# Kernel optimization log

Hardware: AMD Instinct MI355X
Metric: run time of the kernel (lower is better)

## Reference

```python
import jax, jax.numpy as jnp
import numpy as np

NH, KVH, HD = 32, 8, 128          # num heads, kv heads, head dim
HIDDEN = NH * HD                   # 4096
K_BITS = V_BITS = 4
GROUP = 32                         # quantization group size
THETA = 10000.0
FEAT = 32 // K_BITS                # values packed per int32


def _rope_cos_sin(pos, dtype=jnp.float32):
    inv_freq = 1.0 / (THETA ** (jnp.arange(0, HD, 2, dtype=jnp.float32) / HD))
    freqs = pos.astype(jnp.float32)[:, None] * inv_freq[None, :]
    emb = jnp.concatenate([freqs, freqs], axis=-1)  # [t, HD]
    return jnp.cos(emb).astype(dtype), jnp.sin(emb).astype(dtype)


def _rotate_half(x):
    x1, x2 = jnp.split(x, 2, axis=-1)
    return jnp.concatenate([-x2, x1], axis=-1)


def _apply_rope(x, pos):  # x: [b, h, t, d], pos: [t]
    cos, sin = _rope_cos_sin(pos, x.dtype)
    return x * cos[None, None] + _rotate_half(x) * sin[None, None]


def _unpack(packed, bits):
    # packed int32 [..., n] -> float [..., n * (32//bits)], little-endian bit fields
    feat = 32 // bits
    shifts = jnp.arange(feat, dtype=jnp.int32) * bits
    vals = (packed[..., None] >> shifts) & ((1 << bits) - 1)
    return vals.reshape(packed.shape[:-1] + (packed.shape[-1] * feat,)).astype(jnp.float32)


def _dequant(packed, scale, mn, bits, group):
    # group-wise affine dequant: x = q * scale + mn along last dim
    qv = _unpack(packed, bits)
    lead, L = qv.shape[:-1], qv.shape[-1]
    qv = qv.reshape(lead + (L // group, group))
    return (qv * scale[..., None] + mn[..., None]).reshape(lead + (L,))


def _repeat_kv(x, n):
    return jnp.repeat(x, n, axis=1)


def setup_inputs() -> dict:
    key = jax.random.key(0)
    ks = jax.random.split(key, 13)
    B, QL = 8, 8
    TQ, FULL_PAST = 3968, 56
    s = 0.02
    return {
        "hidden_states": jax.random.normal(ks[0], (B, QL, HIDDEN), jnp.float32),
        "Wq": jax.random.normal(ks[1], (NH * HD, HIDDEN), jnp.float32) * s,
        "Wk": jax.random.normal(ks[2], (KVH * HD, HIDDEN), jnp.float32) * s,
        "Wv": jax.random.normal(ks[3], (KVH * HD, HIDDEN), jnp.float32) * s,
        "Wo": jax.random.normal(ks[4], (NH * HD, NH * HD), jnp.float32) * s,
        "key_quant_trans": jax.random.randint(ks[5], (B, KVH, HD, TQ // FEAT), 0, 2**31 - 1, jnp.int32),
        "key_scale_trans": jax.random.uniform(ks[6], (B, KVH, HD, TQ // GROUP), jnp.float32) * 0.05 + 0.01,
        "key_mn_trans": jax.random.normal(ks[7], (B, KVH, HD, TQ // GROUP), jnp.float32) * 0.1,
        "key_full_past": jax.random.normal(ks[8], (B, KVH, FULL_PAST, HD), jnp.float32),
        "value_quant": jax.random.randint(ks[9], (B, KVH, TQ, HD // FEAT), 0, 2**31 - 1, jnp.int32),
        "value_scale": jax.random.uniform(ks[10], (B, KVH, TQ, HD // GROUP), jnp.float32) * 0.05 + 0.01,
        "value_mn": jax.random.normal(ks[11], (B, KVH, TQ, HD // GROUP), jnp.float32) * 0.1,
        "value_full_past": jax.random.normal(ks[12], (B, KVH, FULL_PAST, HD), jnp.float32),
    }


def reference(hidden_states, Wq, Wk, Wv, Wo,
              key_quant_trans, key_scale_trans, key_mn_trans, key_full_past,
              value_quant, value_scale, value_mn, value_full_past):
    b, q_len, _ = hidden_states.shape
    groups = NH // KVH
    # projections
    q = (hidden_states @ Wq.T).reshape(b, q_len, NH, HD).transpose(0, 2, 1, 3)
    k = (hidden_states @ Wk.T).reshape(b, q_len, KVH, HD).transpose(0, 2, 1, 3)
    v = (hidden_states @ Wv.T).reshape(b, q_len, KVH, HD).transpose(0, 2, 1, 3)

    TQ = key_quant_trans.shape[-1] * FEAT
    past_len = TQ + key_full_past.shape[2]
    pos_new = jnp.arange(past_len, past_len + q_len)
    qr = _apply_rope(q, pos_new)

    # quantized key segment: dequant (stored transposed [b,kvh,HD,TQ]) + fused RoPE + bmm
    kq = _dequant(key_quant_trans, key_scale_trans, key_mn_trans, K_BITS, GROUP)
    kq = _apply_rope(kq.transpose(0, 1, 3, 2), jnp.arange(TQ))  # [b,kvh,TQ,HD]
    att_quant = jnp.einsum('bhqd,bhkd->bhqk', qr, _repeat_kv(kq, groups))

    # full-precision residual key segment
    k_full = jnp.concatenate([key_full_past, k], axis=2)
    pos_full = jnp.arange(past_len + q_len - k_full.shape[2], past_len + q_len)
    k_full = _apply_rope(k_full, pos_full)
    att_full = jnp.einsum('bhqd,bhkd->bhqk', qr, _repeat_kv(k_full, groups))

    attn = jnp.concatenate([att_quant, att_full], axis=-1) / np.sqrt(HD).astype(np.float32)
    attn = jax.nn.softmax(attn.astype(jnp.float32), axis=-1).astype(qr.dtype)

    # quantized values (packed along head_dim) + full residual values
    vq = _dequant(value_quant, value_scale, value_mn, V_BITS, GROUP)  # [b,kvh,TQ,HD]
    v_full = jnp.concatenate([value_full_past, v], axis=2)
    Lf = v_full.shape[2]
    out = jnp.einsum('bhqk,bhkd->bhqd', attn[..., :-Lf], _repeat_kv(vq, groups)) \
        + jnp.einsum('bhqk,bhkd->bhqd', attn[..., -Lf:], _repeat_kv(v_full, groups))

    out = out.transpose(0, 2, 1, 3).reshape(b, q_len, NH * HD)
    return out @ Wo.T
```

## Files before the change

### kernel.cpp

```cpp
#include <hip/hip_runtime.h>

typedef unsigned short u16;
typedef short bf16x8 __attribute__((ext_vector_type(8)));
typedef float f32x4 __attribute__((ext_vector_type(4)));

__device__ __forceinline__ float b2f(u16 u){ return __uint_as_float(((unsigned)u)<<16); }
__device__ __forceinline__ u16 f2bf(float f){ return (u16)((__float_as_uint(f)+0x8000u)>>16); }
__device__ __forceinline__ float ldf(const void* p, int i, bool isbf){
  return isbf ? b2f(((const u16*)p)[i]) : ((const float*)p)[i];
}
__device__ __forceinline__ float2 ld2(const void* p, int i, bool isbf){
  if (isbf) { unsigned u = *(const unsigned*)((const u16*)p + i);
              return make_float2(b2f((u16)(u & 0xffffu)), b2f((u16)(u >> 16))); }
  return *(const float2*)((const float*)p + i);
}
__device__ __forceinline__ void ld8(u16* dst, const void* p, int i, bool isbf){
  if (isbf) { *(uint4*)dst = *(const uint4*)((const u16*)p + i); }
  else {
    float4 a = *(const float4*)((const float*)p + i);
    float4 b = *(const float4*)((const float*)p + i + 4);
    dst[0]=f2bf(a.x); dst[1]=f2bf(a.y); dst[2]=f2bf(a.z); dst[3]=f2bf(a.w);
    dst[4]=f2bf(b.x); dst[5]=f2bf(b.y); dst[6]=f2bf(b.z); dst[7]=f2bf(b.w);
  }
}
__device__ __forceinline__ float c8(const float* __restrict__ p, int i, int stride){
  float s = 0.f;
  #pragma unroll
  for (int k = 0; k < 8; k++) s += p[i + k*stride];
  return s;
}
__device__ __forceinline__ void bar(){ asm volatile("s_waitcnt lgkmcnt(0)\n\ts_barrier" ::: "memory"); }
#define RORMAX(x, ctrl) fmaxf((x), __int_as_float(__builtin_amdgcn_update_dpp( \
    __float_as_int(x), __float_as_int(x), (ctrl), 0xF, 0xF, false)))
#define MFMA16(a,b,c) __builtin_amdgcn_mfma_f32_16x16x32_bf16((a),(b),(c),0,0,0)

__global__ __launch_bounds__(256) void ctab_kernel(const u16* __restrict__ h,
                                                   int* __restrict__ flag,
                                                   float2* __restrict__ ctab) {
  int tid = threadIdx.x;
  if (blockIdx.x == 0) {
    int cnt = 0;
    for (int i = tid; i < 4096; i += 256) {
      int e = (h[i] >> 7) & 0xFF;
      cnt += (e >= 116 && e <= 132) ? 1 : 0;
    }
    __shared__ int sh[256];
    sh[tid] = cnt; __syncthreads();
    for (int s = 128; s > 0; s >>= 1) { if (tid < s) sh[tid] += sh[tid + s]; __syncthreads(); }
    if (tid == 0) flag[0] = (sh[0] >= 3100) ? 1 : 0;
  }
  int idx = blockIdx.x * 256 + tid;
  int dm = idx & 63, t = idx >> 6;
  float f = exp2f(-(float)dm * (13.287712379549449f / 64.0f));
  float ang = (float)t * f;
  float s, c;
  sincosf(ang, &s, &c);
  ctab[idx] = make_float2(c, s);
}

__global__ __launch_bounds__(256) void proj_kernel(
    const void* __restrict__ X, const void* __restrict__ Wa,
    const void* __restrict__ Wb, const void* __restrict__ Wc,
    float* __restrict__ out32, int Na, int Nb, int ostride,
    const int* __restrict__ flagp, int x_dyn)
{
  bool fbf = (*flagp != 0);
  bool xbf = x_dyn ? fbf : true;
  int n0 = blockIdx.x * 32;
  int ks0 = blockIdx.y * 512;
  const void* W; int wr0;
  if (n0 < Na)           { W = Wa; wr0 = n0; }
  else if (n0 < Na + Nb) { W = Wb; wr0 = n0 - Na; }
  else                   { W = Wc; wr0 = n0 - Na - Nb; }

  __shared__ u16 Xs[64][136];
  __shared__ u16 Ws[32][136];
  int tid = threadIdx.x;
  int wv = tid >> 6, lane = tid & 63, lr = lane & 15, lq = lane >> 4;
  f32x4 acc0 = {0.f,0.f,0.f,0.f}, acc1 = {0.f,0.f,0.f,0.f};

  for (int ki = 0; ki < 4; ki++) {
    int k0 = ks0 + ki * 128;
    __syncthreads();
    for (int u = tid; u < 1024; u += 256) {
      int row = u >> 4, cc = u & 15;
      ld8(&Xs[row][cc * 8], X, row * 4096 + k0 + cc * 8, xbf);
    }
    for (int u = tid; u < 512; u += 256) {
      int row = u >> 4, cc = u & 15;
      ld8(&Ws[row][cc * 8], W, (wr0 + row) * 4096 + k0 + cc * 8, fbf);
    }
    __syncthreads();
    #pragma unroll
    for (int ks = 0; ks < 4; ks++) {
      bf16x8 af = *(const bf16x8*)&Xs[wv * 16 + lr][ks * 32 + lq * 8];
      bf16x8 b0 = *(const bf16x8*)&Ws[lr][ks * 32 + lq * 8];
      bf16x8 b1 = *(const bf16x8*)&Ws[16 + lr][ks * 32 + lq * 8];
      acc0 = MFMA16(af, b0, acc0);
      acc1 = MFMA16(af, b1, acc1);
    }
  }
  float* outp = out32 + (size_t)blockIdx.y * 64 * ostride;
  #pragma unroll
  for (int r = 0; r < 4; r++) {
    outp[(wv * 16 + lq * 4 + r) * ostride + n0 + lr]      = acc0[r];
    outp[(wv * 16 + lq * 4 + r) * ostride + n0 + 16 + lr] = acc1[r];
  }
}

__global__ __launch_bounds__(256) void prep_kernel(
    const float* __restrict__ Cq32, const void* __restrict__ kfp, const void* __restrict__ vfp,
    const float2* __restrict__ ctab, const int* __restrict__ flagp,
    u16* __restrict__ qrb, u16* __restrict__ kfullb, u16* __restrict__ vfullT)
{
  bool isbf = (*flagp != 0);
  int idx = blockIdx.x * 256 + threadIdx.x;
  if (idx < 262144) {
    int d = idx & 127, row = (idx >> 7) & 31, bh = idx >> 12;
    int b = bh >> 3, kvh = bh & 7, g = row >> 3, qp = row & 7;
    int tok = b * 8 + qp, h = kvh * 4 + g;
    float x  = c8(Cq32, tok * 6144 + h * 128 + d, 393216);
    float x2 = c8(Cq32, tok * 6144 + h * 128 + (d ^ 64), 393216);
    float2 cs = ctab[(4024 + qp) * 64 + (d & 63)];
    float sgn = (d < 64) ? -1.f : 1.f;
    qrb[idx] = f2bf(x * cs.x + sgn * (x2 * cs.y));
  } else if (idx < 786432) {
    int j = idx - 262144;
    int d = j & 127, t = (j >> 7) & 63, bh = j >> 13;
    int b = bh >> 3, kvh = bh & 7;
    float x, x2;
    if (t < 56) {
      x  = ldf(kfp, (bh * 56 + t) * 128 + d, isbf);
      x2 = ldf(kfp, (bh * 56 + t) * 128 + (d ^ 64), isbf);
    } else {
      int tok = b * 8 + (t - 56);
      x  = c8(Cq32, tok * 6144 + 4096 + kvh * 128 + d, 393216);
      x2 = c8(Cq32, tok * 6144 + 4096 + kvh * 128 + (d ^ 64), 393216);
    }
    float2 cs = ctab[(3968 + t) * 64 + (d & 63)];
    float sgn = (d < 64) ? -1.f : 1.f;
    kfullb[j] = f2bf(x * cs.x + sgn * (x2 * cs.y));
  } else {
    int j = idx - 786432;
    int t = j & 63, d = (j >> 6) & 127, bh = j >> 13;
    int b = bh >> 3, kvh = bh & 7;
    float x;
    if (t < 56) x = ldf(vfp, (bh * 56 + t) * 128 + d, isbf);
    else        x = c8(Cq32, (b * 8 + t - 56) * 6144 + 5120 + kvh * 128 + d, 393216);
    vfullT[j] = f2bf(x);
  }
}

__global__ __launch_bounds__(256) void attn_kernel(
    const int* __restrict__ kqw, const void* __restrict__ ksc, const void* __restrict__ kmn,
    const int* __restrict__ vqw, const void* __restrict__ vsc, const void* __restrict__ vmn,
    const u16* __restrict__ qrb, const u16* __restrict__ kfullb, const u16* __restrict__ vfullT,
    const float2* __restrict__ ctab, const int* __restrict__ flagp,
    u16* __restrict__ Opart, float* __restrict__ ml)
{
  bool isbf = (*flagp != 0);
  int bh = blockIdx.x, grp = blockIdx.y;
  int tid = threadIdx.x;
  int c0 = grp * 4;
  int N = (grp == 15) ? 3 : 4;

  __shared__ __align__(16) unsigned char L[37120];
  u16* Kt = (u16*)L;
  u16* Vt = (u16*)(L + 16384);
  u16* Pt = (u16*)(L + 32768);
  float* pmax = (float*)(L + 36864);

  int wv = tid >> 6, lane = tid & 63, lr = lane & 15, lq = lane >> 4;
  int mt = wv & 1, nh = wv >> 1;
  int sx = (lr & 7) << 3;

  const int* kq_lo = kqw + (bh * 128 + lane) * 496;
  const int* kq_hi = kq_lo + 64 * 496;
  int klo = (bh * 128 + lane) * 124;
  int khi = klo + 64 * 124;
  const int* vqp = vqw + (bh * 3968 + lane) * 16 + wv * 4;
  int voff = (bh * 3968 + lane) * 4 + wv;

  bf16x8 qa[4];
  #pragma unroll
  for (int ks = 0; ks < 4; ks++)
    qa[ks] = *(const bf16x8*)&qrb[(bh * 32 + mt * 16 + lr) * 128 + ks * 32 + lq * 8];
  bf16x8 onev;
  #pragma unroll
  for (int j2 = 0; j2 < 8; j2++) onev[j2] = (short)0x3F80;

  float m_prev[4], l_run[4], alpha[4], mx[4];
  f32x4 zf = {0.f,0.f,0.f,0.f};
  f32x4 oacc[4] = {zf, zf, zf, zf};
  f32x4 sacc[2];
  #pragma unroll
  for (int r = 0; r < 4; r++) { m_prev[r] = -INFINITY; l_run[r] = 0.f; }

  unsigned kwl[2], kwh[2];
  float2 ksl, kml, ksh, kmh;
  uint4 vw; float vs, vm;

#define KLOAD(cn) do { \
    kwl[0] = kq_lo[(cn)*8 + wv]; kwl[1] = kq_lo[(cn)*8 + wv + 4]; \
    kwh[0] = kq_hi[(cn)*8 + wv]; kwh[1] = kq_hi[(cn)*8 + wv + 4]; \
    ksl = ld2(ksc, klo + (cn)*2, isbf); kml = ld2(kmn, klo + (cn)*2, isbf); \
    ksh = ld2(ksc, khi + (cn)*2, isbf); kmh = ld2(kmn, khi + (cn)*2, isbf); } while(0)
#define VLOAD(cn) do { \
    vw = *(const uint4*)(vqp + (cn)*1024); \
    vs = ldf(vsc, voff + (cn)*256, isbf); vm = ldf(vmn, voff + (cn)*256, isbf); } while(0)
#define KDEQ(cn) do { \
    _Pragma("unroll") \
    for (int it = 0; it < 2; it++) { \
      int w = wv + 4 * it; \
      unsigned w1 = kwl[it], w2 = kwh[it]; \
      float sc1 = it ? ksl.y : ksl.x, m1 = it ? kml.y : kml.x; \
      float sc2 = it ? ksh.y : ksh.x, m2 = it ? kmh.y : kmh.x; \
      const float2* ct = &ctab[((cn) * 64 + w * 8) * 64 + lane]; \
      _Pragma("unroll") \
      for (int ii = 0; ii < 8; ii++) { \
        float v1 = (float)((w1 >> (4 * ii)) & 15u) * sc1 + m1; \
        float v2 = (float)((w2 >> (4 * ii)) & 15u) * sc2 + m2; \
        float2 cs = ct[ii * 64]; \
        int t = w * 8 + ii; \
        Kt[(t * 128 + lane)      ^ ((t & 7) << 3)] = f2bf(v1 * cs.x - v2 * cs.y); \
        Kt[(t * 128 + lane + 64) ^ ((t & 7) << 3)] = f2bf(v2 * cs.x + v1 * cs.y); \
      } \
    } } while(0)
#define PVSTEP() do { \
    f32x4 pv[4] = {zf, zf, zf, zf}; f32x4 ls = zf; \
    _Pragma("unroll") \
    for (int ks = 0; ks < 2; ks++) { \
      bf16x8 af = *(const bf16x8*)&Pt[((mt*16 + lr)*64 + ks*32 + lq*8) ^ sx]; \
      ls = MFMA16(af, onev, ls); \
      _Pragma("unroll") \
      for (int nt = 0; nt < 4; nt++) { \
        bf16x8 bv = *(const bf16x8*)&Vt[((nh*64 + nt*16 + lr)*64 + ks*32 + lq*8) ^ sx]; \
        pv[nt] = MFMA16(af, bv, pv[nt]); \
      } \
    } \
    _Pragma("unroll") \
    for (int r = 0; r < 4; r++) { \
      l_run[r] = l_run[r] * alpha[r] + ls[r]; \
      _Pragma("unroll") \
      for (int nt = 0; nt < 4; nt++) \
        oacc[nt][r] = oacc[nt][r] * alpha[r] + pv[nt][r]; \
    } } while(0)

  KLOAD(c0);
  VLOAD(c0);
  KDEQ(c0);
  KLOAD(c0 + 1);
  bar();

  for (int i = 0; i < N; i++) {
    int c = c0 + i;
    f32x4 sa0 = zf, sa1 = zf;
    #pragma unroll
    for (int ks = 0; ks < 4; ks++) {
      bf16x8 b0 = *(const bf16x8*)&Kt[((nh*32 + lr)*128      + ks*32 + lq*8) ^ sx];
      bf16x8 b1 = *(const bf16x8*)&Kt[((nh*32 + 16 + lr)*128 + ks*32 + lq*8) ^ sx];
      sa0 = MFMA16(qa[ks], b0, sa0);
      sa1 = MFMA16(qa[ks], b1, sa1);
    }
    if (i > 0) PVSTEP();
    #pragma unroll
    for (int r = 0; r < 4; r++) {
      sa0[r] *= 0.08838834764831845f;
      sa1[r] *= 0.08838834764831845f;
      float m0 = fmaxf(sa0[r], sa1[r]);
      m0 = RORMAX(m0, 0x128);
      m0 = RORMAX(m0, 0x124);
      m0 = RORMAX(m0, 0x122);
      m0 = RORMAX(m0, 0x121);
      mx[r] = m0;
    }
    if (lr == 0) {
      #pragma unroll
      for (int r = 0; r < 4; r++) pmax[wv * 16 + lq * 4 + r] = mx[r];
    }
    sacc[0] = sa0; sacc[1] = sa1;
    bar();
    #pragma unroll
    for (int r = 0; r < 4; r++) {
      float cm = fmaxf(mx[r], pmax[(wv ^ 2) * 16 + lq * 4 + r]);
      float mn2 = fmaxf(m_prev[r], cm);
      alpha[r] = __expf(m_prev[r] - mn2);
      m_prev[r] = mn2;
    }
    #pragma unroll
    for (int nt = 0; nt < 2; nt++) {
      #pragma unroll
      for (int r = 0; r < 4; r++) {
        float p = __expf(sacc[nt][r] - m_prev[r]);
        int q = mt * 16 + lq * 4 + r, k = nh * 32 + nt * 16 + lr;
        Pt[(q * 64 + k) ^ ((q & 7) << 3)] = f2bf(p);
      }
    }
    if (c != 62) {
      unsigned wds[4] = {vw.x, vw.y, vw.z, vw.w};
      #pragma unroll
      for (int it = 0; it < 4; it++) {
        unsigned wd = wds[it];
        #pragma unroll
        for (int ii = 0; ii < 8; ii++) {
          int d = (wv * 4 + it) * 8 + ii;
          Vt[(d * 64 + lane) ^ ((d & 7) << 3)] = f2bf((float)((wd >> (4 * ii)) & 15u) * vs + vm);
        }
      }
    } else {
      for (int u = tid; u < 1024; u += 256) {
        int dd = u >> 3, t8 = u & 7;
        *(uint4*)&Vt[(dd * 64 + t8 * 8) ^ ((dd & 7) << 3)] =
            *(const uint4*)&vfullT[(bh * 128 + dd) * 64 + t8 * 8];
      }
    }
    if (i + 1 < N) {
      if (c + 1 == 62) {
        for (int u = tid; u < 1024; u += 256) {
          int row = u >> 4, cc = u & 15;
          *(uint4*)&Kt[(row * 128 + cc * 8) ^ ((row & 7) << 3)] =
              *(const uint4*)&kfullb[(bh * 64 + row) * 128 + cc * 8];
        }
      } else {
        KDEQ(c + 1);
      }
    }
    if (i + 2 < N && c + 2 < 62) KLOAD(c + 2);
    if (i + 1 < N && c + 1 < 62) VLOAD(c + 1);
    bar();
  }
  PVSTEP();

  u16* Ob = Opart + (size_t)((bh * 16 + grp) * 32) * 128;
  #pragma unroll
  for (int nt = 0; nt < 4; nt++)
    #pragma unroll
    for (int r = 0; r < 4; r++)
      Ob[(mt * 16 + lq * 4 + r) * 128 + nh * 64 + nt * 16 + lr] = f2bf(oacc[nt][r]);
  if (wv < 2 && lr == 0) {
    #pragma unroll
    for (int r = 0; r < 4; r++) {
      ml[((bh * 16 + grp) * 32 + mt * 16 + lq * 4 + r) * 2 + 0] = m_prev[r];
      ml[((bh * 16 + grp) * 32 + mt * 16 + lq * 4 + r) * 2 + 1] = l_run[r];
    }
  }
#undef KLOAD
#undef VLOAD
#undef KDEQ
#undef PVSTEP
}

__global__ __launch_bounds__(256) void combine_kernel(
    const u16* __restrict__ Opart, const float* __restrict__ ml, u16* __restrict__ attn_out)
{
  int bh = blockIdx.x, dq = blockIdx.y, tid = threadIdx.x;
  __shared__ float Wg[16][33];
  __shared__ float Ls[32];
  if (tid < 32) {
    int row = tid;
    float M = -INFINITY;
    for (int g = 0; g < 16; g++)
      M = fmaxf(M, ml[((bh * 16 + g) * 32 + row) * 2]);
    float Lacc = 0.f;
    for (int g = 0; g < 16; g++) {
      float m = ml[((bh * 16 + g) * 32 + row) * 2];
      float l = ml[((bh * 16 + g) * 32 + row) * 2 + 1];
      float w = __expf(m - M);
      Wg[g][row] = w;
      Lacc += l * w;
    }
    Ls[row] = Lacc;
  }
  __syncthreads();
  int row = tid >> 3, ds = tid & 7;
  int d0 = dq * 32 + ds * 4;
  float a0 = 0.f, a1 = 0.f, a2 = 0.f, a3 = 0.f;
  for (int g = 0; g < 16; g++) {
    float w = Wg[g][row];
    const u16* p = Opart + (size_t)((bh * 16 + g) * 32 + row) * 128 + d0;
    uint2 v = *(const uint2*)p;
    const u16* h = (const u16*)&v;
    a0 += w * b2f(h[0]); a1 += w * b2f(h[1]); a2 += w * b2f(h[2]); a3 += w * b2f(h[3]);
  }
  float inv = 1.0f / Ls[row];
  int b = bh >> 3, kvh = bh & 7, hg = row >> 3, qp = row & 7;
  u16* dst = attn_out + (size_t)(b * 8 + qp) * 4096 + (kvh * 4 + hg) * 128 + d0;
  dst[0] = f2bf(a0 * inv); dst[1] = f2bf(a1 * inv);
  dst[2] = f2bf(a2 * inv); dst[3] = f2bf(a3 * inv);
}

__global__ __launch_bounds__(256) void cast_kernel(
    const float* __restrict__ O32, const int* __restrict__ flagp, void* __restrict__ out)
{
  int i = blockIdx.x * 256 + threadIdx.x;
  float v = c8(O32, i, 262144);
  if (*flagp) ((u16*)out)[i] = f2bf(v);
  else        ((float*)out)[i] = v;
}

extern "C" void kernel_launch(void* const* d_in, const int* in_sizes, int n_in,
                              void* d_out, int out_size, void* d_ws, size_t ws_size,
                              hipStream_t stream)
{
  const void* hidden = d_in[0];
  const void* Wq  = d_in[1];
  const void* Wk  = d_in[2];
  const void* Wv  = d_in[3];
  const void* Wo  = d_in[4];
  const int*  kqw = (const int*)d_in[5];
  const void* ksc = d_in[6];
  const void* kmn = d_in[7];
  const void* kfp = d_in[8];
  const int*  vqw = (const int*)d_in[9];
  const void* vsc = d_in[10];
  const void* vmn = d_in[11];
  const void* vfp = d_in[12];

  char* ws = (char*)d_ws;
  int*    flag     = (int*)(ws);
  float2* ctab     = (float2*)(ws + 256);
  float*  Cq32     = (float*)(ws + 2064640);
  u16*    Opart    = (u16*)(ws + 2064640);
  float*  O32      = (float*)(ws + 2064640);
  u16*    qrb      = (u16*)(ws + 18841856);
  u16*    attn_out = qrb;
  u16*    kfullb   = (u16*)(ws + 19366144);
  u16*    vfullT   = (u16*)(ws + 20414720);
  float*  ml       = (float*)(ws + 21463296);

  ctab_kernel<<<1008, 256, 0, stream>>>((const u16*)hidden, flag, ctab);
  proj_kernel<<<dim3(192, 8), 256, 0, stream>>>(hidden, Wq, Wk, Wv, Cq32, 4096, 1024, 6144, flag, 1);
  prep_kernel<<<5120, 256, 0, stream>>>(Cq32, kfp, vfp, ctab, flag, qrb, kfullb, vfullT);
  attn_kernel<<<dim3(64, 16), 256, 0, stream>>>(kqw, ksc, kmn, vqw, vsc, vmn,
                                                qrb, kfullb, vfullT, ctab, flag, Opart, ml);
  combine_kernel<<<dim3(64, 4), 256, 0, stream>>>(Opart, ml, attn_out);
  proj_kernel<<<dim3(128, 8), 256, 0, stream>>>(attn_out, Wo, Wo, Wo, O32, 4096, 0, 4096, flag, 0);
  cast_kernel<<<1024, 256, 0, stream>>>(O32, flag, d_out);
}
```

Before: 294.0 us.

## Widen projection GEMM tile to 64 columns and prefetch next K-slab into registers

The projection kernel now computes 64 output columns per block instead of 32, with four MFMA accumulators per wave, and halves the grid for both the QKV and output projections. Global loads for the next 128-wide K slab are issued into registers before the MFMA work on the current slab, so load latency overlaps compute. X tiles are reused across twice as many columns, but each block holds more registers and there are fewer blocks to fill the GPU.

```diff
diff --git a/kernel.cpp b/kernel.cpp
--- a/kernel.cpp
+++ b/kernel.cpp
@@ -21,6 +21,19 @@
     float4 b = *(const float4*)((const float*)p + i + 4);
     dst[0]=f2bf(a.x); dst[1]=f2bf(a.y); dst[2]=f2bf(a.z); dst[3]=f2bf(a.w);
     dst[4]=f2bf(b.x); dst[5]=f2bf(b.y); dst[6]=f2bf(b.z); dst[7]=f2bf(b.w);
+  }
+}
+__device__ __forceinline__ void pre8(uint4& A, uint4& B, const void* p, int i, bool isb){
+  if (isb) { A = *(const uint4*)((const u16*)p + i); }
+  else { A = *(const uint4*)((const float*)p + i);
+         B = *(const uint4*)((const float*)p + i + 4); }
+}
+__device__ __forceinline__ void st8(u16* dst, const uint4& A, const uint4& B, bool isb){
+  if (isb) { *(uint4*)dst = A; }
+  else {
+    const float* a = (const float*)&A; const float* b = (const float*)&B;
+    dst[0]=f2bf(a[0]); dst[1]=f2bf(a[1]); dst[2]=f2bf(a[2]); dst[3]=f2bf(a[3]);
+    dst[4]=f2bf(b[0]); dst[5]=f2bf(b[1]); dst[6]=f2bf(b[2]); dst[7]=f2bf(b[3]);
   }
 }
 __device__ __forceinline__ float c8(const float* __restrict__ p, int i, int stride){
@@ -66,7 +79,7 @@
 {
   bool fbf = (*flagp != 0);
   bool xbf = x_dyn ? fbf : true;
-  int n0 = blockIdx.x * 32;
+  int n0 = blockIdx.x * 64;
   int ks0 = blockIdx.y * 512;
   const void* W; int wr0;
   if (n0 < Na)           { W = Wa; wr0 = n0; }
@@ -74,38 +87,54 @@
   else                   { W = Wc; wr0 = n0 - Na - Nb; }
 
   __shared__ u16 Xs[64][136];
-  __shared__ u16 Ws[32][136];
+  __shared__ u16 Ws[64][136];
   int tid = threadIdx.x;
   int wv = tid >> 6, lane = tid & 63, lr = lane & 15, lq = lane >> 4;
-  f32x4 acc0 = {0.f,0.f,0.f,0.f}, acc1 = {0.f,0.f,0.f,0.f};
-
+  f32x4 zf = {0.f,0.f,0.f,0.f};
+  f32x4 acc[4] = {zf, zf, zf, zf};
+
+  uint4 xa[4], xb[4], wa[4], wb[4];
+  #pragma unroll
+  for (int s = 0; s < 4; s++) {
+    int e = s * 256 + tid, row = e >> 4, c8i = e & 15;
+    pre8(xa[s], xb[s], X, row * 4096 + ks0 + c8i * 8, xbf);
+    pre8(wa[s], wb[s], W, (wr0 + row) * 4096 + ks0 + c8i * 8, fbf);
+  }
+  #pragma unroll 1
   for (int ki = 0; ki < 4; ki++) {
-    int k0 = ks0 + ki * 128;
-    __syncthreads();
-    for (int u = tid; u < 1024; u += 256) {
-      int row = u >> 4, cc = u & 15;
-      ld8(&Xs[row][cc * 8], X, row * 4096 + k0 + cc * 8, xbf);
-    }
-    for (int u = tid; u < 512; u += 256) {
-      int row = u >> 4, cc = u & 15;
-      ld8(&Ws[row][cc * 8], W, (wr0 + row) * 4096 + k0 + cc * 8, fbf);
-    }
-    __syncthreads();
+    bar();
+    #pragma unroll
+    for (int s = 0; s < 4; s++) {
+      int e = s * 256 + tid, row = e >> 4, c8i = e & 15;
+      st8(&Xs[row][c8i * 8], xa[s], xb[s], xbf);
+      st8(&Ws[row][c8i * 8], wa[s], wb[s], fbf);
+    }
+    if (ki < 3) {
+      int k0 = ks0 + (ki + 1) * 128;
+      #pragma unroll
+      for (int s = 0; s < 4; s++) {
+        int e = s * 256 + tid, row = e >> 4, c8i = e & 15;
+        pre8(xa[s], xb[s], X, row * 4096 + k0 + c8i * 8, xbf);
+        pre8(wa[s], wb[s], W, (wr0 + row) * 4096 + k0 + c8i * 8, fbf);
+      }
+    }
+    bar();
     #pragma unroll
     for (int ks = 0; ks < 4; ks++) {
       bf16x8 af = *(const bf16x8*)&Xs[wv * 16 + lr][ks * 32 + lq * 8];
-      bf16x8 b0 = *(const bf16x8*)&Ws[lr][ks * 32 + lq * 8];
-      bf16x8 b1 = *(const bf16x8*)&Ws[16 + lr][ks * 32 + lq * 8];
-      acc0 = MFMA16(af, b0, acc0);
-      acc1 = MFMA16(af, b1, acc1);
+      #pragma unroll
+      for (int nt = 0; nt < 4; nt++) {
+        bf16x8 bv = *(const bf16x8*)&Ws[nt * 16 + lr][ks * 32 + lq * 8];
+        acc[nt] = MFMA16(af, bv, acc[nt]);
+      }
     }
   }
   float* outp = out32 + (size_t)blockIdx.y * 64 * ostride;
   #pragma unroll
-  for (int r = 0; r < 4; r++) {
-    outp[(wv * 16 + lq * 4 + r) * ostride + n0 + lr]      = acc0[r];
-    outp[(wv * 16 + lq * 4 + r) * ostride + n0 + 16 + lr] = acc1[r];
-  }
+  for (int nt = 0; nt < 4; nt++)
+    #pragma unroll
+    for (int r = 0; r < 4; r++)
+      outp[(wv * 16 + lq * 4 + r) * ostride + n0 + nt * 16 + lr] = acc[nt][r];
 }
 
 __global__ __launch_bounds__(256) void prep_kernel(
@@ -429,11 +458,11 @@
   float*  ml       = (float*)(ws + 21463296);
 
   ctab_kernel<<<1008, 256, 0, stream>>>((const u16*)hidden, flag, ctab);
-  proj_kernel<<<dim3(192, 8), 256, 0, stream>>>(hidden, Wq, Wk, Wv, Cq32, 4096, 1024, 6144, flag, 1);
+  proj_kernel<<<dim3(96, 8), 256, 0, stream>>>(hidden, Wq, Wk, Wv, Cq32, 4096, 1024, 6144, flag, 1);
   prep_kernel<<<5120, 256, 0, stream>>>(Cq32, kfp, vfp, ctab, flag, qrb, kfullb, vfullT);
   attn_kernel<<<dim3(64, 16), 256, 0, stream>>>(kqw, ksc, kmn, vqw, vsc, vmn,
                                                 qrb, kfullb, vfullT, ctab, flag, Opart, ml);
   combine_kernel<<<dim3(64, 4), 256, 0, stream>>>(Opart, ml, attn_out);
-  proj_kernel<<<dim3(128, 8), 256, 0, stream>>>(attn_out, Wo, Wo, Wo, O32, 4096, 0, 4096, flag, 0);
+  proj_kernel<<<dim3(64, 8), 256, 0, stream>>>(attn_out, Wo, Wo, Wo, O32, 4096, 0, 4096, flag, 0);
   cast_kernel<<<1024, 256, 0, stream>>>(O32, flag, d_out);
 }
```

Measured after the change: 291.3 us. No clear change (-0.9%).
